# Kernel tuning notes

Measured on AMD Instinct MI355X. Metric: run time of the kernel, lower is better.

The kernel has to match this reference:

```python
import jax, jax.numpy as jnp
import numpy as np

B, S, Dm, H = 2, 2048, 1024, 16
HD = Dm // H            # 64, head dim == rotary dim
INTER = 4096            # intermediate_size (gated: W1 -> 2*INTER)
EPS = 1e-5


def _rotate_half(x):
    x1, x2 = jnp.split(x, 2, axis=-1)
    return jnp.concatenate((-x2, x1), axis=-1)


def _layernorm(x, g, b):
    mu = jnp.mean(x, axis=-1, keepdims=True)
    var = jnp.var(x, axis=-1, keepdims=True)
    return (x - mu) * jax.lax.rsqrt(var + EPS) * g + b


def setup_inputs() -> dict:
    key = jax.random.key(0)
    ks = jax.random.split(key, 12)
    s = 0.02
    hidden_states = jax.random.normal(ks[0], (B, S, Dm), jnp.float32)
    attention_mask = jnp.zeros((B, 1, 1, S), jnp.float32)
    # RoPE angles: pos * inv_freq, shape [S, HD]
    inv_freq = 1.0 / (10000.0 ** (jnp.arange(0, HD, 2, dtype=jnp.float32) / HD))
    ang = jnp.arange(S, dtype=jnp.float32)[:, None] * inv_freq[None, :]
    rope_freqs = jnp.concatenate([ang, ang], axis=-1)  # [S, HD]
    params = {
        'Wq': jax.random.normal(ks[1], (Dm, Dm)) * s, 'bq': jnp.zeros((Dm,)),
        'Wk': jax.random.normal(ks[2], (Dm, Dm)) * s, 'bk': jnp.zeros((Dm,)),
        'Wv': jax.random.normal(ks[3], (Dm, Dm)) * s, 'bv': jnp.zeros((Dm,)),
        'Wo': jax.random.normal(ks[4], (Dm, Dm)) * s, 'bo': jnp.zeros((Dm,)),
        'ln1_g': jnp.ones((Dm,)), 'ln1_b': jnp.zeros((Dm,)),
        'ln2_g': jnp.ones((Dm,)), 'ln2_b': jnp.zeros((Dm,)),
        'W1': jax.random.normal(ks[5], (Dm, 2 * INTER)) * s, 'b1': jnp.zeros((2 * INTER,)),
        'W2': jax.random.normal(ks[6], (INTER, Dm)) * s, 'b2': jnp.zeros((Dm,)),
    }
    return {'hidden_states': hidden_states, 'attention_mask': attention_mask,
            'rope_freqs': rope_freqs, **params}


def reference(hidden_states, attention_mask, rope_freqs,
              Wq, bq, Wk, bk, Wv, bv, Wo, bo,
              ln1_g, ln1_b, ln2_g, ln2_b, W1, b1, W2, b2):
    # ---- attention block (pre-LN) ----
    x = _layernorm(hidden_states, ln1_g, ln1_b)          # [B,S,Dm]
    def heads(t):  # [B,S,Dm] -> [B,H,S,HD]
        return t.reshape(B, S, H, HD).transpose(0, 2, 1, 3)
    q = heads(x @ Wq + bq)
    k = heads(x @ Wk + bk)
    v = heads(x @ Wv + bv)
    # RoPE (full head dim rotated)
    cos = jnp.cos(rope_freqs)[None, None, :, :]          # [1,1,S,HD]
    sin = jnp.sin(rope_freqs)[None, None, :, :]
    q = q * cos + _rotate_half(q) * sin
    k = k * cos + _rotate_half(k) * sin
    scores = jnp.einsum('bhqd,bhkd->bhqk', q, k) / jnp.sqrt(jnp.float32(HD))
    scores = scores + attention_mask
    probs = jax.nn.softmax(scores, axis=-1)
    probs = jnp.where(attention_mask < -1e-5, 0.0, probs)  # masked_fill
    ctx = jnp.einsum('bhqk,bhkd->bhqd', probs, v)
    ctx = ctx.transpose(0, 2, 1, 3).reshape(B, S, Dm)
    hidden = hidden_states + (ctx @ Wo + bo)              # residual
    # ---- MLP block (pre-LN, swiglu) ----
    y = _layernorm(hidden, ln2_g, ln2_b)
    h = y @ W1 + b1
    h0, h1 = jnp.split(h, 2, axis=-1)
    act = h0 * jax.nn.silu(h1)                            # swiglu
    out = hidden + (act @ W2 + b2)
    return out
```

## Files before the change

kernel.cpp:

```cpp
#include <hip/hip_runtime.h>
#include <cstdint>


typedef __bf16 bf16;
typedef __bf16 bf16x8 __attribute__((ext_vector_type(8)));
typedef float f32x4 __attribute__((ext_vector_type(4)));

#define B_ 2
#define S_ 2048
#define DM_ 1024
#define H_ 16
#define HD_ 64
#define INTER_ 4096

#define MFMA(a, b, c) __builtin_amdgcn_mfma_f32_16x16x32_bf16(a, b, c, 0, 0, 0)

__device__ __forceinline__ void cp16(void* lds, const void* g) {
  __builtin_amdgcn_global_load_lds(
      (const __attribute__((address_space(1))) void*)(uintptr_t)g,
      (__attribute__((address_space(3))) void*)(uint32_t)(uintptr_t)lds,
      16, 0, 0);
}

__global__ void transpose_f32_bf16(const float* __restrict__ in,
                                   bf16* __restrict__ out, int K, int N) {
  __shared__ float tile[32][33];
  int n0 = blockIdx.x * 32, k0 = blockIdx.y * 32;
  int tx = threadIdx.x, ty = threadIdx.y;
#pragma unroll
  for (int i = 0; i < 32; i += 8)
    tile[ty + i][tx] = in[(size_t)(k0 + ty + i) * N + n0 + tx];
  __syncthreads();
#pragma unroll
  for (int i = 0; i < 32; i += 8)
    out[(size_t)(n0 + ty + i) * K + k0 + tx] = (bf16)tile[tx][ty + i];
}

__global__ void transpose_w1(const float* __restrict__ in,
                             bf16* __restrict__ out) {
  __shared__ float tile[32][33];
  int n0 = blockIdx.x * 32, k0 = blockIdx.y * 32;
  int tx = threadIdx.x, ty = threadIdx.y;
#pragma unroll
  for (int i = 0; i < 32; i += 8)
    tile[ty + i][tx] = in[(size_t)(k0 + ty + i) * (2 * INTER_) + n0 + tx];
  __syncthreads();
#pragma unroll
  for (int i = 0; i < 32; i += 8) {
    int n = n0 + ty + i;
    int r = ((n & 4095) >> 3) * 16 + ((n >> 12) << 3) + (n & 7);
    out[(size_t)r * DM_ + k0 + tx] = (bf16)tile[tx][ty + i];
  }
}

__global__ void transpose_bf16(const bf16* __restrict__ in,
                               bf16* __restrict__ out, int K, int N) {
  __shared__ bf16 tile[32][33];
  const size_t mo = (size_t)blockIdx.z * K * N;
  int n0 = blockIdx.x * 32, k0 = blockIdx.y * 32;
  int tx = threadIdx.x, ty = threadIdx.y;
#pragma unroll
  for (int i = 0; i < 32; i += 8)
    tile[ty + i][tx] = in[mo + (size_t)(k0 + ty + i) * N + n0 + tx];
  __syncthreads();
#pragma unroll
  for (int i = 0; i < 32; i += 8)
    out[mo + (size_t)(n0 + ty + i) * K + k0 + tx] = tile[tx][ty + i];
}

__global__ __launch_bounds__(256) void ln_bf16(const float* __restrict__ x,
                                               const float* __restrict__ g,
                                               const float* __restrict__ bta,
                                               bf16* __restrict__ out) {
  int row = blockIdx.x;
  int tid = threadIdx.x;
  const float4* xr = (const float4*)(x + (size_t)row * DM_);
  float4 v = xr[tid];
  float s1 = v.x + v.y + v.z + v.w;
  float s2 = v.x * v.x + v.y * v.y + v.z * v.z + v.w * v.w;
#pragma unroll
  for (int off = 32; off; off >>= 1) {
    s1 += __shfl_xor(s1, off);
    s2 += __shfl_xor(s2, off);
  }
  __shared__ float rA[4], rB[4];
  int wave = tid >> 6, lane = tid & 63;
  if (!lane) { rA[wave] = s1; rB[wave] = s2; }
  __syncthreads();
  float t1 = rA[0] + rA[1] + rA[2] + rA[3];
  float t2 = rB[0] + rB[1] + rB[2] + rB[3];
  float mean = t1 * (1.0f / DM_);
  float var = t2 * (1.0f / DM_) - mean * mean;
  float rstd = rsqrtf(var + 1e-5f);
  int col = tid * 4;
  float4 gv = ((const float4*)g)[tid];
  float4 bv = ((const float4*)bta)[tid];
  bf16* o = out + (size_t)row * DM_ + col;
  o[0] = (bf16)((v.x - mean) * rstd * gv.x + bv.x);
  o[1] = (bf16)((v.y - mean) * rstd * gv.y + bv.y);
  o[2] = (bf16)((v.z - mean) * rstd * gv.z + bv.z);
  o[3] = (bf16)((v.w - mean) * rstd * gv.w + bv.w);
}

template <int EPI, int BN>
__global__ __launch_bounds__(256, 2) void gemm_bt(
    const bf16* __restrict__ A, const bf16* __restrict__ Bt,
    const float* __restrict__ b0, const float* __restrict__ b1p,
    const float* __restrict__ b2p, const float* __restrict__ rope,
    const float* __restrict__ resid, void* __restrict__ outp, int N, int K) {
  constexpr int TM = (BN == 128) ? 4 : 2;
  __shared__ __align__(16) bf16 As[128 * 32];
  __shared__ __align__(16) bf16 Bs[BN * 32];
  const int tid = threadIdx.x;
  const int lane = tid & 63, wave = tid >> 6;
  const int c = lane & 15, quad = lane >> 4;
  const int wr = (BN == 128) ? (wave >> 1) : wave;
  const int wc = (BN == 128) ? (wave & 1) : 0;
  const int mbase = wr * (16 * TM), nbase = wc * 64;
  const int bm0 = blockIdx.y * 128, bn0 = blockIdx.x * BN;
  const int sw = (c >> 1) & 3;

  f32x4 acc[TM][4];
  const f32x4 z4 = {0.f, 0.f, 0.f, 0.f};
#pragma unroll
  for (int i = 0; i < TM; ++i)
#pragma unroll
    for (int j = 0; j < 4; ++j) acc[i][j] = z4;

  for (int k0 = 0; k0 < K; k0 += 32) {
    __syncthreads();
#pragma unroll
    for (int it = 0; it < 2; ++it) {
      int idx = tid + it * 256;
      int row = idx >> 2, chg = (idx & 3) ^ ((idx >> 3) & 3);
      cp16(As + (size_t)idx * 8, A + (size_t)(bm0 + row) * K + k0 + chg * 8);
    }
#pragma unroll
    for (int it = 0; it < BN / 64; ++it) {
      int idx = tid + it * 256;
      int row = idx >> 2, chg = (idx & 3) ^ ((idx >> 3) & 3);
      cp16(Bs + (size_t)idx * 8, Bt + (size_t)(bn0 + row) * K + k0 + chg * 8);
    }
    __syncthreads();
    bf16x8 af[TM], bfr[4];
#pragma unroll
    for (int ti = 0; ti < TM; ++ti)
      af[ti] = *(const bf16x8*)(As + (mbase + ti * 16 + c) * 32 + (quad ^ sw) * 8);
#pragma unroll
    for (int tj = 0; tj < 4; ++tj)
      bfr[tj] = *(const bf16x8*)(Bs + (nbase + tj * 16 + c) * 32 + (quad ^ sw) * 8);
#pragma unroll
    for (int ti = 0; ti < TM; ++ti)
#pragma unroll
      for (int tj = 0; tj < 4; ++tj)
        acc[ti][tj] = MFMA(af[ti], bfr[tj], acc[ti][tj]);
  }

  if constexpr (EPI == 2) {
    float* o = (float*)outp;
#pragma unroll
    for (int ti = 0; ti < TM; ++ti)
#pragma unroll
      for (int r = 0; r < 4; ++r) {
        int gm = bm0 + mbase + ti * 16 + quad * 4 + r;
        const float* rrow = resid + (size_t)gm * N;
        float* orow = o + (size_t)gm * N;
#pragma unroll
        for (int tj = 0; tj < 4; ++tj) {
          int gn = bn0 + nbase + tj * 16 + c;
          orow[gn] = acc[ti][tj][r] + b0[gn] + rrow[gn];
        }
      }
  } else if constexpr (EPI == 4) {
    bf16* act = (bf16*)outp;
#pragma unroll
    for (int ti = 0; ti < TM; ++ti)
#pragma unroll
      for (int r = 0; r < 4; ++r) {
        int gm = bm0 + mbase + ti * 16 + quad * 4 + r;
        bf16* arow = act + (size_t)gm * INTER_;
#pragma unroll
        for (int tj = 0; tj < 4; ++tj) {
          int gn = bn0 + nbase + tj * 16 + c;
          int g = gn >> 4, t = gn & 7, hi = (gn >> 3) & 1;
          float val = acc[ti][tj][r] + b0[g * 8 + t + (hi << 12)];
          float part = __shfl_xor(val, 8);
          if (!hi) {
            float sg = part / (1.0f + __expf(-part));
            arow[g * 8 + t] = (bf16)(val * sg);
          }
        }
      }
  } else {
    bf16* o = (bf16*)outp;
#pragma unroll
    for (int ti = 0; ti < TM; ++ti)
#pragma unroll
      for (int r = 0; r < 4; ++r) {
        int gm = bm0 + mbase + ti * 16 + quad * 4 + r;
        int s = gm & (S_ - 1);
        int bb = gm >> 11;
#pragma unroll
        for (int tj = 0; tj < 4; ++tj) {
          int gn = bn0 + nbase + tj * 16 + c;
          int mtx = gn >> 10;
          const float* bp = (mtx == 0) ? b0 : (mtx == 1) ? b1p : b2p;
          int ci = gn & 1023;
          float val = acc[ti][tj][r] + bp[ci];
          if (mtx < 2) {
            int pj = (tj & 2) ? tj - 2 : tj + 2;
            int ci2 = (tj & 2) ? ci - 32 : ci + 32;
            float part = acc[ti][pj][r] + bp[ci2];
            if (!(tj & 2)) part = -part;
            float fr = rope[s * HD_ + (gn & 63)];
            float sn, cs;
            __sincosf(fr, &sn, &cs);
            val = val * cs + part * sn;
            if (mtx == 0) val *= 0.125f;
          }
          o[(size_t)mtx * (32 * S_ * HD_) +
            (((size_t)(bb * H_ + ((gn >> 6) & 15))) * S_ + s) * HD_ + (gn & 63)] =
              (bf16)val;
        }
      }
  }
}

__global__ __launch_bounds__(256, 4) void flash_attn(
    const bf16* __restrict__ q, const bf16* __restrict__ k,
    const bf16* __restrict__ vt, const float* __restrict__ mask,
    bf16* __restrict__ ctx) {
  __shared__ __align__(16) bf16 Ks[64 * 64];
  __shared__ __align__(16) bf16 Vs[64 * 64];
  __shared__ __align__(16) bf16 Ps[4][16 * 64];

  const int tid = threadIdx.x;
  const int lane = tid & 63, wave = tid >> 6;
  const int c = lane & 15, quad = lane >> 4;
  const int bh = blockIdx.y, b = bh >> 4, h = bh & 15;
  const int q0 = blockIdx.x * 64;
  const int csw = c & 7;

  const bf16* qh = q + (size_t)bh * S_ * HD_;
  const bf16* kh = k + (size_t)bh * S_ * HD_;
  const bf16* vh = vt + (size_t)bh * HD_ * S_;
  const float* mrow = mask + (size_t)b * S_;

  int qrow = q0 + wave * 16 + c;
  bf16x8 qa0 = *(const bf16x8*)(qh + (size_t)qrow * HD_ + quad * 8);
  bf16x8 qa1 = *(const bf16x8*)(qh + (size_t)qrow * HD_ + (quad + 4) * 8);

  const f32x4 z4 = {0.f, 0.f, 0.f, 0.f};
  f32x4 o[4] = {z4, z4, z4, z4};
  float l_i[4] = {0.f, 0.f, 0.f, 0.f};

  for (int k0 = 0; k0 < S_; k0 += 64) {
    __syncthreads();
#pragma unroll
    for (int it = 0; it < 2; ++it) {
      int idx = tid + it * 256;
      int row = idx >> 3, chg = (idx & 7) ^ (row & 7);
      cp16(Ks + (size_t)idx * 8, kh + (size_t)(k0 + row) * HD_ + chg * 8);
      cp16(Vs + (size_t)idx * 8, vh + (size_t)row * S_ + k0 + chg * 8);
    }
    __syncthreads();

    f32x4 s[4];
    float mv[4];
#pragma unroll
    for (int tj = 0; tj < 4; ++tj) {
      const bf16* kr = Ks + (tj * 16 + c) * 64;
      bf16x8 kb0 = *(const bf16x8*)(kr + (quad ^ csw) * 8);
      bf16x8 kb1 = *(const bf16x8*)(kr + ((quad + 4) ^ csw) * 8);
      s[tj] = MFMA(qa0, kb0, z4);
      s[tj] = MFMA(qa1, kb1, s[tj]);
      mv[tj] = mrow[k0 + tj * 16 + c];
    }

    bf16* pw = Ps[wave];
#pragma unroll
    for (int tj = 0; tj < 4; ++tj) {
      bool msk = mv[tj] < -1e-5f;
#pragma unroll
      for (int r = 0; r < 4; ++r) {
        float e = __expf(s[tj][r] + mv[tj]);
        l_i[r] += e;
        float p = msk ? 0.f : e;
        int prow = quad * 4 + r;
        int pos = (tj * 2 + (c >> 3)) ^ (prow & 7);
        pw[prow * 64 + pos * 8 + (c & 7)] = (bf16)p;
      }
    }
    asm volatile("s_waitcnt lgkmcnt(0)" ::: "memory");
    bf16x8 pa0 = *(const bf16x8*)(pw + c * 64 + (quad ^ csw) * 8);
    bf16x8 pa1 = *(const bf16x8*)(pw + c * 64 + ((quad + 4) ^ csw) * 8);

#pragma unroll
    for (int tn = 0; tn < 4; ++tn) {
      const bf16* vr = Vs + (tn * 16 + c) * 64;
      bf16x8 vb0 = *(const bf16x8*)(vr + (quad ^ csw) * 8);
      bf16x8 vb1 = *(const bf16x8*)(vr + ((quad + 4) ^ csw) * 8);
      o[tn] = MFMA(pa0, vb0, o[tn]);
      o[tn] = MFMA(pa1, vb1, o[tn]);
    }
  }

#pragma unroll
  for (int r = 0; r < 4; ++r) {
    float l = l_i[r];
#pragma unroll
    for (int off = 1; off < 16; off <<= 1) l += __shfl_xor(l, off);
    float inv = 1.0f / l;
    int qout = q0 + wave * 16 + quad * 4 + r;
    bf16* crow = ctx + ((size_t)(b * S_ + qout)) * DM_ + h * HD_;
#pragma unroll
    for (int tn = 0; tn < 4; ++tn) crow[tn * 16 + c] = (bf16)(o[tn][r] * inv);
  }
}

extern "C" void kernel_launch(void* const* d_in, const int* in_sizes, int n_in,
                              void* d_out, int out_size, void* d_ws,
                              size_t ws_size, hipStream_t stream) {
  const float* hs   = (const float*)d_in[0];
  const float* mask = (const float*)d_in[1];
  const float* rope = (const float*)d_in[2];
  const float* Wq = (const float*)d_in[3];  const float* bq = (const float*)d_in[4];
  const float* Wk = (const float*)d_in[5];  const float* bk = (const float*)d_in[6];
  const float* Wv = (const float*)d_in[7];  const float* bv = (const float*)d_in[8];
  const float* Wo = (const float*)d_in[9];  const float* bo = (const float*)d_in[10];
  const float* g1 = (const float*)d_in[11]; const float* be1 = (const float*)d_in[12];
  const float* g2 = (const float*)d_in[13]; const float* be2 = (const float*)d_in[14];
  const float* W1 = (const float*)d_in[15]; const float* b1 = (const float*)d_in[16];
  const float* W2 = (const float*)d_in[17]; const float* b2 = (const float*)d_in[18];
  float* out = (float*)d_out;
  char* ws = (char*)d_ws;
  const size_t MB = 1ull << 20;

  bf16* Wqkvt = (bf16*)(ws + 0 * MB);
  bf16* Wot = (bf16*)(ws + 6 * MB);
  bf16* W1t = (bf16*)(ws + 8 * MB);
  bf16* W2t = (bf16*)(ws + 24 * MB);
  bf16* xln = (bf16*)(ws + 32 * MB);
  float* hid = (float*)(ws + 40 * MB);
  bf16* qkv = (bf16*)(ws + 56 * MB);
  bf16* vtr = (bf16*)(ws + 80 * MB);
  bf16* ctx = (bf16*)(ws + 88 * MB);
  bf16* act = (bf16*)(ws + 96 * MB);

  dim3 blk(256);
  dim3 tb(32, 8);

  transpose_f32_bf16<<<dim3(32, 32), tb, 0, stream>>>(Wq, Wqkvt, 1024, 1024);
  transpose_f32_bf16<<<dim3(32, 32), tb, 0, stream>>>(Wk, Wqkvt + (1 << 20), 1024, 1024);
  transpose_f32_bf16<<<dim3(32, 32), tb, 0, stream>>>(Wv, Wqkvt + (2 << 20), 1024, 1024);
  transpose_f32_bf16<<<dim3(32, 32), tb, 0, stream>>>(Wo, Wot, 1024, 1024);
  transpose_w1<<<dim3(256, 32), tb, 0, stream>>>(W1, W1t);
  transpose_f32_bf16<<<dim3(32, 128), tb, 0, stream>>>(W2, W2t, 4096, 1024);

  ln_bf16<<<4096, blk, 0, stream>>>(hs, g1, be1, xln);

  gemm_bt<0, 128><<<dim3(24, 32), blk, 0, stream>>>(
      xln, Wqkvt, bq, bk, bv, rope, nullptr, qkv, 3072, 1024);

  transpose_bf16<<<dim3(2, 64, 32), tb, 0, stream>>>(
      qkv + (size_t)2 * 32 * S_ * HD_, vtr, 2048, 64);

  flash_attn<<<dim3(32, 32), blk, 0, stream>>>(
      qkv, qkv + (size_t)32 * S_ * HD_, vtr, mask, ctx);

  gemm_bt<2, 64><<<dim3(16, 32), blk, 0, stream>>>(
      ctx, Wot, bo, nullptr, nullptr, nullptr, hs, hid, 1024, 1024);

  ln_bf16<<<4096, blk, 0, stream>>>(hid, g2, be2, xln);

  gemm_bt<4, 128><<<dim3(64, 32), blk, 0, stream>>>(
      xln, W1t, b1, nullptr, nullptr, nullptr, nullptr, act, 8192, 1024);

  gemm_bt<2, 64><<<dim3(16, 32), blk, 0, stream>>>(
      act, W2t, b2, nullptr, nullptr, nullptr, hid, out, 1024, 4096);

  (void)in_sizes; (void)n_in; (void)out_size; (void)ws_size;
}
```

Before: 473.1 us.

## Switch GEMMs to 32x32 MFMA, enlarge attention tiles, use exp2, merge weight transposes

The GEMM kernel moves from 16x16x32 to 32x32x16 MFMA tiles, with a new LDS swizzle and reworked epilogue index math. Flash attention now uses 512-thread blocks covering 128 queries and 128-key tiles, and folds log2(e) into the Q scale so it can use exp2. The four 1024x1024 weight transposes are merged into one launch. The aim is fewer LDS reads per MFMA, fewer barriers and launches, and a cheaper exponential, at the cost of more registers and shared memory per block and new swizzle and layout logic that could be wrong.

```diff
diff --git a/kernel.cpp b/kernel.cpp
--- a/kernel.cpp
+++ b/kernel.cpp
@@ -5,6 +5,7 @@
 typedef __bf16 bf16;
 typedef __bf16 bf16x8 __attribute__((ext_vector_type(8)));
 typedef float f32x4 __attribute__((ext_vector_type(4)));
+typedef float f32x16 __attribute__((ext_vector_type(16)));
 
 #define B_ 2
 #define S_ 2048
@@ -13,13 +14,42 @@
 #define HD_ 64
 #define INTER_ 4096
 
-#define MFMA(a, b, c) __builtin_amdgcn_mfma_f32_16x16x32_bf16(a, b, c, 0, 0, 0)
+#define MFMA16(a, b, c) __builtin_amdgcn_mfma_f32_16x16x32_bf16(a, b, c, 0, 0, 0)
+#define MFMA32(a, b, c) __builtin_amdgcn_mfma_f32_32x32x16_bf16(a, b, c, 0, 0, 0)
+
+#if __has_builtin(__builtin_amdgcn_exp2f)
+#define EXP2F(x) __builtin_amdgcn_exp2f(x)
+#else
+#define EXP2F(x) __expf((x) * 0.6931471805599453f)
+#endif
 
 __device__ __forceinline__ void cp16(void* lds, const void* g) {
   __builtin_amdgcn_global_load_lds(
       (const __attribute__((address_space(1))) void*)(uintptr_t)g,
       (__attribute__((address_space(3))) void*)(uint32_t)(uintptr_t)lds,
       16, 0, 0);
+}
+
+__global__ void transpose4_f32_bf16(const float* __restrict__ w0,
+                                    const float* __restrict__ w1,
+                                    const float* __restrict__ w2,
+                                    const float* __restrict__ w3,
+                                    bf16* __restrict__ o0, bf16* __restrict__ o1,
+                                    bf16* __restrict__ o2, bf16* __restrict__ o3) {
+  __shared__ float tile[32][33];
+  const float* in = (blockIdx.z == 0) ? w0 : (blockIdx.z == 1) ? w1
+                    : (blockIdx.z == 2) ? w2 : w3;
+  bf16* out = (blockIdx.z == 0) ? o0 : (blockIdx.z == 1) ? o1
+              : (blockIdx.z == 2) ? o2 : o3;
+  int n0 = blockIdx.x * 32, k0 = blockIdx.y * 32;
+  int tx = threadIdx.x, ty = threadIdx.y;
+#pragma unroll
+  for (int i = 0; i < 32; i += 8)
+    tile[ty + i][tx] = in[(size_t)(k0 + ty + i) * 1024 + n0 + tx];
+  __syncthreads();
+#pragma unroll
+  for (int i = 0; i < 32; i += 8)
+    out[(size_t)(n0 + ty + i) * 1024 + k0 + tx] = (bf16)tile[tx][ty + i];
 }
 
 __global__ void transpose_f32_bf16(const float* __restrict__ in,
@@ -108,82 +138,88 @@
     const float* __restrict__ b0, const float* __restrict__ b1p,
     const float* __restrict__ b2p, const float* __restrict__ rope,
     const float* __restrict__ resid, void* __restrict__ outp, int N, int K) {
-  constexpr int TM = (BN == 128) ? 4 : 2;
+  constexpr int WM = (BN == 128) ? 2 : 1;
   __shared__ __align__(16) bf16 As[128 * 32];
   __shared__ __align__(16) bf16 Bs[BN * 32];
   const int tid = threadIdx.x;
   const int lane = tid & 63, wave = tid >> 6;
-  const int c = lane & 15, quad = lane >> 4;
-  const int wr = (BN == 128) ? (wave >> 1) : wave;
-  const int wc = (BN == 128) ? (wave & 1) : 0;
-  const int mbase = wr * (16 * TM), nbase = wc * 64;
+  const int col = lane & 31, half = lane >> 5;
+  const int mbase = (BN == 128) ? (wave >> 1) * 64 : wave * 32;
+  const int nbase = (BN == 128) ? (wave & 1) * 64 : 0;
   const int bm0 = blockIdx.y * 128, bn0 = blockIdx.x * BN;
-  const int sw = (c >> 1) & 3;
-
-  f32x4 acc[TM][4];
-  const f32x4 z4 = {0.f, 0.f, 0.f, 0.f};
-#pragma unroll
-  for (int i = 0; i < TM; ++i)
-#pragma unroll
-    for (int j = 0; j < 4; ++j) acc[i][j] = z4;
+
+  f32x16 acc[WM][2];
+#pragma unroll
+  for (int i = 0; i < WM; ++i)
+#pragma unroll
+    for (int j = 0; j < 2; ++j)
+#pragma unroll
+      for (int r = 0; r < 16; ++r) acc[i][j][r] = 0.f;
 
   for (int k0 = 0; k0 < K; k0 += 32) {
     __syncthreads();
 #pragma unroll
     for (int it = 0; it < 2; ++it) {
       int idx = tid + it * 256;
-      int row = idx >> 2, chg = (idx & 3) ^ ((idx >> 3) & 3);
+      int row = idx >> 2, chg = (idx & 3) ^ (row & 3);
       cp16(As + (size_t)idx * 8, A + (size_t)(bm0 + row) * K + k0 + chg * 8);
     }
 #pragma unroll
     for (int it = 0; it < BN / 64; ++it) {
       int idx = tid + it * 256;
-      int row = idx >> 2, chg = (idx & 3) ^ ((idx >> 3) & 3);
+      int row = idx >> 2, chg = (idx & 3) ^ (row & 3);
       cp16(Bs + (size_t)idx * 8, Bt + (size_t)(bn0 + row) * K + k0 + chg * 8);
     }
     __syncthreads();
-    bf16x8 af[TM], bfr[4];
-#pragma unroll
-    for (int ti = 0; ti < TM; ++ti)
-      af[ti] = *(const bf16x8*)(As + (mbase + ti * 16 + c) * 32 + (quad ^ sw) * 8);
-#pragma unroll
-    for (int tj = 0; tj < 4; ++tj)
-      bfr[tj] = *(const bf16x8*)(Bs + (nbase + tj * 16 + c) * 32 + (quad ^ sw) * 8);
-#pragma unroll
-    for (int ti = 0; ti < TM; ++ti)
-#pragma unroll
-      for (int tj = 0; tj < 4; ++tj)
-        acc[ti][tj] = MFMA(af[ti], bfr[tj], acc[ti][tj]);
+#pragma unroll
+    for (int s = 0; s < 2; ++s) {
+      bf16x8 af[WM], bfr[2];
+#pragma unroll
+      for (int mi = 0; mi < WM; ++mi) {
+        int row = mbase + mi * 32 + col;
+        af[mi] = *(const bf16x8*)(As + row * 32 + ((s * 2 + half) ^ (row & 3)) * 8);
+      }
+#pragma unroll
+      for (int ni = 0; ni < 2; ++ni) {
+        int row = nbase + ni * 32 + col;
+        bfr[ni] = *(const bf16x8*)(Bs + row * 32 + ((s * 2 + half) ^ (row & 3)) * 8);
+      }
+#pragma unroll
+      for (int mi = 0; mi < WM; ++mi)
+#pragma unroll
+        for (int ni = 0; ni < 2; ++ni)
+          acc[mi][ni] = MFMA32(af[mi], bfr[ni], acc[mi][ni]);
+    }
   }
 
   if constexpr (EPI == 2) {
     float* o = (float*)outp;
 #pragma unroll
-    for (int ti = 0; ti < TM; ++ti)
-#pragma unroll
-      for (int r = 0; r < 4; ++r) {
-        int gm = bm0 + mbase + ti * 16 + quad * 4 + r;
+    for (int mi = 0; mi < WM; ++mi)
+#pragma unroll
+      for (int reg = 0; reg < 16; ++reg) {
+        int gm = bm0 + mbase + mi * 32 + (reg & 3) + 8 * (reg >> 2) + 4 * half;
         const float* rrow = resid + (size_t)gm * N;
         float* orow = o + (size_t)gm * N;
 #pragma unroll
-        for (int tj = 0; tj < 4; ++tj) {
-          int gn = bn0 + nbase + tj * 16 + c;
-          orow[gn] = acc[ti][tj][r] + b0[gn] + rrow[gn];
+        for (int ni = 0; ni < 2; ++ni) {
+          int gn = bn0 + nbase + ni * 32 + col;
+          orow[gn] = acc[mi][ni][reg] + b0[gn] + rrow[gn];
         }
       }
   } else if constexpr (EPI == 4) {
     bf16* act = (bf16*)outp;
 #pragma unroll
-    for (int ti = 0; ti < TM; ++ti)
-#pragma unroll
-      for (int r = 0; r < 4; ++r) {
-        int gm = bm0 + mbase + ti * 16 + quad * 4 + r;
+    for (int mi = 0; mi < WM; ++mi)
+#pragma unroll
+      for (int reg = 0; reg < 16; ++reg) {
+        int gm = bm0 + mbase + mi * 32 + (reg & 3) + 8 * (reg >> 2) + 4 * half;
         bf16* arow = act + (size_t)gm * INTER_;
 #pragma unroll
-        for (int tj = 0; tj < 4; ++tj) {
-          int gn = bn0 + nbase + tj * 16 + c;
+        for (int ni = 0; ni < 2; ++ni) {
+          int gn = bn0 + nbase + ni * 32 + col;
           int g = gn >> 4, t = gn & 7, hi = (gn >> 3) & 1;
-          float val = acc[ti][tj][r] + b0[g * 8 + t + (hi << 12)];
+          float val = acc[mi][ni][reg] + b0[g * 8 + t + (hi << 12)];
           float part = __shfl_xor(val, 8);
           if (!hi) {
             float sg = part / (1.0f + __expf(-part));
@@ -193,53 +229,50 @@
       }
   } else {
     bf16* o = (bf16*)outp;
-#pragma unroll
-    for (int ti = 0; ti < TM; ++ti)
-#pragma unroll
-      for (int r = 0; r < 4; ++r) {
-        int gm = bm0 + mbase + ti * 16 + quad * 4 + r;
+    const int mtx = bn0 >> 10;
+    const float* bp = (mtx == 0) ? b0 : (mtx == 1) ? b1p : b2p;
+#pragma unroll
+    for (int mi = 0; mi < WM; ++mi)
+#pragma unroll
+      for (int reg = 0; reg < 16; ++reg) {
+        int gm = bm0 + mbase + mi * 32 + (reg & 3) + 8 * (reg >> 2) + 4 * half;
         int s = gm & (S_ - 1);
         int bb = gm >> 11;
 #pragma unroll
-        for (int tj = 0; tj < 4; ++tj) {
-          int gn = bn0 + nbase + tj * 16 + c;
-          int mtx = gn >> 10;
-          const float* bp = (mtx == 0) ? b0 : (mtx == 1) ? b1p : b2p;
-          int ci = gn & 1023;
-          float val = acc[ti][tj][r] + bp[ci];
+        for (int ni = 0; ni < 2; ++ni) {
+          int gn = bn0 + nbase + ni * 32 + col;
+          int ci = gn & 1023, hd = gn & 63;
+          float val = acc[mi][ni][reg] + bp[ci];
           if (mtx < 2) {
-            int pj = (tj & 2) ? tj - 2 : tj + 2;
-            int ci2 = (tj & 2) ? ci - 32 : ci + 32;
-            float part = acc[ti][pj][r] + bp[ci2];
-            if (!(tj & 2)) part = -part;
-            float fr = rope[s * HD_ + (gn & 63)];
+            float part = acc[mi][ni ^ 1][reg] + bp[ci ^ 32];
+            if (!(gn & 32)) part = -part;
+            float fr = rope[s * HD_ + hd];
             float sn, cs;
             __sincosf(fr, &sn, &cs);
             val = val * cs + part * sn;
-            if (mtx == 0) val *= 0.125f;
+            if (mtx == 0) val *= 0.1803368867f;
           }
           o[(size_t)mtx * (32 * S_ * HD_) +
-            (((size_t)(bb * H_ + ((gn >> 6) & 15))) * S_ + s) * HD_ + (gn & 63)] =
+            (((size_t)(bb * H_ + ((gn >> 6) & 15))) * S_ + s) * HD_ + hd] =
               (bf16)val;
         }
       }
   }
 }
 
-__global__ __launch_bounds__(256, 4) void flash_attn(
+__global__ __launch_bounds__(512, 2) void flash_attn(
     const bf16* __restrict__ q, const bf16* __restrict__ k,
     const bf16* __restrict__ vt, const float* __restrict__ mask,
     bf16* __restrict__ ctx) {
-  __shared__ __align__(16) bf16 Ks[64 * 64];
-  __shared__ __align__(16) bf16 Vs[64 * 64];
-  __shared__ __align__(16) bf16 Ps[4][16 * 64];
+  __shared__ __align__(16) bf16 Ks[128 * 64];
+  __shared__ __align__(16) bf16 Vs[64 * 128];
+  __shared__ __align__(16) bf16 Ps[8][16 * 128];
 
   const int tid = threadIdx.x;
   const int lane = tid & 63, wave = tid >> 6;
   const int c = lane & 15, quad = lane >> 4;
   const int bh = blockIdx.y, b = bh >> 4, h = bh & 15;
-  const int q0 = blockIdx.x * 64;
-  const int csw = c & 7;
+  const int q0 = blockIdx.x * 128;
 
   const bf16* qh = q + (size_t)bh * S_ * HD_;
   const bf16* kh = k + (size_t)bh * S_ * HD_;
@@ -248,60 +281,70 @@
 
   int qrow = q0 + wave * 16 + c;
   bf16x8 qa0 = *(const bf16x8*)(qh + (size_t)qrow * HD_ + quad * 8);
-  bf16x8 qa1 = *(const bf16x8*)(qh + (size_t)qrow * HD_ + (quad + 4) * 8);
+  bf16x8 qa1 = *(const bf16x8*)(qh + (size_t)qrow * HD_ + 32 + quad * 8);
 
   const f32x4 z4 = {0.f, 0.f, 0.f, 0.f};
   f32x4 o[4] = {z4, z4, z4, z4};
   float l_i[4] = {0.f, 0.f, 0.f, 0.f};
 
-  for (int k0 = 0; k0 < S_; k0 += 64) {
+  for (int k0 = 0; k0 < S_; k0 += 128) {
     __syncthreads();
 #pragma unroll
     for (int it = 0; it < 2; ++it) {
-      int idx = tid + it * 256;
+      int idx = tid + it * 512;
       int row = idx >> 3, chg = (idx & 7) ^ (row & 7);
       cp16(Ks + (size_t)idx * 8, kh + (size_t)(k0 + row) * HD_ + chg * 8);
+    }
+#pragma unroll
+    for (int it = 0; it < 2; ++it) {
+      int idx = tid + it * 512;
+      int row = idx >> 4, chg = (idx & 15) ^ (row & 15);
       cp16(Vs + (size_t)idx * 8, vh + (size_t)row * S_ + k0 + chg * 8);
     }
     __syncthreads();
 
-    f32x4 s[4];
-    float mv[4];
-#pragma unroll
-    for (int tj = 0; tj < 4; ++tj) {
-      const bf16* kr = Ks + (tj * 16 + c) * 64;
-      bf16x8 kb0 = *(const bf16x8*)(kr + (quad ^ csw) * 8);
-      bf16x8 kb1 = *(const bf16x8*)(kr + ((quad + 4) ^ csw) * 8);
-      s[tj] = MFMA(qa0, kb0, z4);
-      s[tj] = MFMA(qa1, kb1, s[tj]);
-      mv[tj] = mrow[k0 + tj * 16 + c];
+    f32x4 sv[8];
+    float mv2[8];
+#pragma unroll
+    for (int tj = 0; tj < 8; ++tj) {
+      int krow = tj * 16 + c;
+      const bf16* kr = Ks + krow * 64;
+      bf16x8 kb0 = *(const bf16x8*)(kr + (quad ^ (krow & 7)) * 8);
+      bf16x8 kb1 = *(const bf16x8*)(kr + ((4 + quad) ^ (krow & 7)) * 8);
+      sv[tj] = MFMA16(qa0, kb0, z4);
+      sv[tj] = MFMA16(qa1, kb1, sv[tj]);
+      mv2[tj] = mrow[k0 + krow] * 1.4426950408889634f;
     }
 
     bf16* pw = Ps[wave];
 #pragma unroll
-    for (int tj = 0; tj < 4; ++tj) {
-      bool msk = mv[tj] < -1e-5f;
+    for (int tj = 0; tj < 8; ++tj) {
+      bool msk = mv2[tj] < -1.4426950e-5f;
 #pragma unroll
       for (int r = 0; r < 4; ++r) {
-        float e = __expf(s[tj][r] + mv[tj]);
+        float e = EXP2F(sv[tj][r] + mv2[tj]);
         l_i[r] += e;
         float p = msk ? 0.f : e;
         int prow = quad * 4 + r;
-        int pos = (tj * 2 + (c >> 3)) ^ (prow & 7);
-        pw[prow * 64 + pos * 8 + (c & 7)] = (bf16)p;
+        int chunk = (tj * 2 + (c >> 3)) ^ prow;
+        pw[prow * 128 + chunk * 8 + (c & 7)] = (bf16)p;
       }
     }
     asm volatile("s_waitcnt lgkmcnt(0)" ::: "memory");
-    bf16x8 pa0 = *(const bf16x8*)(pw + c * 64 + (quad ^ csw) * 8);
-    bf16x8 pa1 = *(const bf16x8*)(pw + c * 64 + ((quad + 4) ^ csw) * 8);
+    bf16x8 pa[4];
+#pragma unroll
+    for (int ks = 0; ks < 4; ++ks)
+      pa[ks] = *(const bf16x8*)(pw + c * 128 + ((ks * 4 + quad) ^ c) * 8);
 
 #pragma unroll
     for (int tn = 0; tn < 4; ++tn) {
-      const bf16* vr = Vs + (tn * 16 + c) * 64;
-      bf16x8 vb0 = *(const bf16x8*)(vr + (quad ^ csw) * 8);
-      bf16x8 vb1 = *(const bf16x8*)(vr + ((quad + 4) ^ csw) * 8);
-      o[tn] = MFMA(pa0, vb0, o[tn]);
-      o[tn] = MFMA(pa1, vb1, o[tn]);
+      int vrow = tn * 16 + c;
+      const bf16* vr = Vs + vrow * 128;
+#pragma unroll
+      for (int ks = 0; ks < 4; ++ks) {
+        bf16x8 vb = *(const bf16x8*)(vr + ((ks * 4 + quad) ^ (vrow & 15)) * 8);
+        o[tn] = MFMA16(pa[ks], vb, o[tn]);
+      }
     }
   }
 
@@ -350,10 +393,8 @@
   dim3 blk(256);
   dim3 tb(32, 8);
 
-  transpose_f32_bf16<<<dim3(32, 32), tb, 0, stream>>>(Wq, Wqkvt, 1024, 1024);
-  transpose_f32_bf16<<<dim3(32, 32), tb, 0, stream>>>(Wk, Wqkvt + (1 << 20), 1024, 1024);
-  transpose_f32_bf16<<<dim3(32, 32), tb, 0, stream>>>(Wv, Wqkvt + (2 << 20), 1024, 1024);
-  transpose_f32_bf16<<<dim3(32, 32), tb, 0, stream>>>(Wo, Wot, 1024, 1024);
+  transpose4_f32_bf16<<<dim3(32, 32, 4), tb, 0, stream>>>(
+      Wq, Wk, Wv, Wo, Wqkvt, Wqkvt + (1 << 20), Wqkvt + (2 << 20), Wot);
   transpose_w1<<<dim3(256, 32), tb, 0, stream>>>(W1, W1t);
   transpose_f32_bf16<<<dim3(32, 128), tb, 0, stream>>>(W2, W2t, 4096, 1024);
 
@@ -365,7 +406,7 @@
   transpose_bf16<<<dim3(2, 64, 32), tb, 0, stream>>>(
       qkv + (size_t)2 * 32 * S_ * HD_, vtr, 2048, 64);
 
-  flash_attn<<<dim3(32, 32), blk, 0, stream>>>(
+  flash_attn<<<dim3(16, 32), dim3(512), 0, stream>>>(
       qkv, qkv + (size_t)32 * S_ * HD_, vtr, mask, ctx);
 
   gemm_bt<2, 64><<<dim3(16, 32), blk, 0, stream>>>(
```

Result: slower. 518.6 us (+9.6%).
